# Kernel tuning notes

Measured on AMD Instinct MI355X. Metric: run time of the kernel, lower is better.

The kernel has to match this reference:

```python
import jax, jax.numpy as jnp
import numpy as np

FEATURE_DIM = 128
NUM_EDGES = 640000
NUM_NODES = 40000


def setup_inputs() -> dict:
    key = jax.random.key(0)
    ks = jax.random.split(key, 10)
    d = FEATURE_DIM
    scale = 1.0 / np.sqrt(d)
    inp = {
        "messages": jax.random.normal(ks[0], (NUM_EDGES, d), dtype=jnp.float32),
        "receivers": jax.random.randint(ks[1], (NUM_EDGES,), 0, NUM_NODES, dtype=jnp.int32),
        "num_segments": NUM_NODES,
        "Wk": jax.random.normal(ks[2], (d, d), dtype=jnp.float32) * scale,
        "bk": jnp.zeros((d,), dtype=jnp.float32),
        "Wv": jax.random.normal(ks[3], (d, d), dtype=jnp.float32) * scale,
        "bv": jnp.zeros((d,), dtype=jnp.float32),
        "Wq": jax.random.normal(ks[4], (d, d), dtype=jnp.float32) * scale,
        "bq": jnp.zeros((d,), dtype=jnp.float32),
        "Wo": jax.random.normal(ks[5], (d, d), dtype=jnp.float32) * scale,
        "bo": jnp.zeros((d,), dtype=jnp.float32),
    }
    return inp


def reference(messages, receivers, num_segments, Wk, bk, Wv, bv, Wq, bq, Wo, bo):
    d = messages.shape[-1]
    # per-edge key/value projections
    keys = messages @ Wk + bk            # [E, d]
    values = messages @ Wv + bv          # [E, d]
    # node-level summed messages -> queries
    summed = jax.ops.segment_sum(messages, receivers, num_segments)  # [N, d]
    queries = summed @ Wq + bq                                       # [N, d]
    # scalar attention score per edge (dot over full feature dim)
    msg_q = queries[receivers]                                       # [E, d]
    scores = jnp.sum(msg_q * keys, axis=-1) / jnp.sqrt(jnp.float32(d))  # [E]
    # segment softmax over edges sharing a receiver
    max_s = jax.ops.segment_max(scores, receivers, num_segments)     # [N]
    exp_s = jnp.exp(scores - max_s[receivers])                       # [E]
    sum_e = jax.ops.segment_sum(exp_s, receivers, num_segments)      # [N]
    attn = exp_s / (sum_e[receivers] + 1e-08)                        # [E]
    # weighted scatter-sum of values, then output projection
    agg = jax.ops.segment_sum(values * attn[:, None], receivers, num_segments)  # [N, d]
    return agg @ Wo + bo
```

## Files before the change

kernel.cpp:

```cpp
#include <hip/hip_runtime.h>

#define D 128
#define RSQRT_D 0.088388347648318440550f
#define NEG_HUGE -3.4e38f

#define FMA4(acc, s, b) { acc.x += (s)*(b).x; acc.y += (s)*(b).y; acc.z += (s)*(b).z; acc.w += (s)*(b).w; }

__global__ __launch_bounds__(256) void prep_kernel(
    const float* __restrict__ Wq, const float* __restrict__ Wk,
    const float* __restrict__ bq, const float* __restrict__ bk,
    const float* __restrict__ Wv, const float* __restrict__ Wo,
    const float* __restrict__ bv,
    float* __restrict__ Wqk, float* __restrict__ bqk,
    float* __restrict__ wqb, float* __restrict__ bqb,
    float* __restrict__ Wvo, float* __restrict__ bvo,
    int* __restrict__ zbase, int zcount) {
    int bid = blockIdx.x, t = threadIdx.x;
    if (bid < 64) {
        int i = bid * 2 + (t >> 7), j = t & 127;
        float a1 = 0.f, a2 = 0.f;
        for (int u = 0; u < D; ++u) {
            a1 += Wq[i * D + u] * Wk[j * D + u];
            a2 += Wv[i * D + u] * Wo[u * D + j];
        }
        Wqk[i * D + j] = a1;
        Wvo[i * D + j] = a2;
    } else if (bid == 64) {
        if (t < D) {
            int j = t;
            float a1 = 0.f, a2 = 0.f, a3 = 0.f;
            for (int u = 0; u < D; ++u) {
                a1 += bq[u] * Wk[j * D + u];
                a2 += Wq[j * D + u] * bk[u];
                a3 += bv[u] * Wo[u * D + j];
            }
            bqk[j] = a1; wqb[j] = a2; bvo[j] = a3;
            if (j == 0) {
                float b = 0.f;
                for (int u = 0; u < D; ++u) b += bq[u] * bk[u];
                *bqb = b;
            }
        }
    } else {
        int idx = (bid - 65) * 256 + t;
        if (idx < zcount) zbase[idx] = 0;
    }
}

__global__ void hist_kernel(const int* __restrict__ recv, int* __restrict__ cnt, int E) {
    int e = blockIdx.x * blockDim.x + threadIdx.x;
    if (e >= E) return;
    atomicAdd(&cnt[recv[e]], 1);
}

__global__ __launch_bounds__(1024) void scan_kernel(const int* __restrict__ cnt,
                                                    int* __restrict__ start, int N) {
    __shared__ int wsum[16];
    __shared__ int chunk_total;
    int t = threadIdx.x;
    int w = t >> 6, lane = t & 63;
    int running = 0;
    for (int base = 0; base <= N; base += 1024) {
        int i = base + t;
        int v = (i < N) ? cnt[i] : 0;
        int x = v;
#pragma unroll
        for (int off = 1; off < 64; off <<= 1) {
            int y = __shfl_up(x, off);
            if (lane >= off) x += y;
        }
        if (lane == 63) wsum[w] = x;
        __syncthreads();
        if (w == 0 && lane < 16) {
            int s = wsum[lane];
#pragma unroll
            for (int off = 1; off < 16; off <<= 1) {
                int y = __shfl_up(s, off);
                if (lane >= off) s += y;
            }
            wsum[lane] = s;
            if (lane == 15) chunk_total = s;
        }
        __syncthreads();
        int waveoff = (w == 0) ? 0 : wsum[w - 1];
        if (i <= N) start[i] = running + waveoff + x - v;
        running += chunk_total;
        __syncthreads();
    }
}

__global__ void fill_kernel(const int* __restrict__ recv, const int* __restrict__ start,
                            int* __restrict__ cursor, int* __restrict__ eidx, int E) {
    int e = blockIdx.x * blockDim.x + threadIdx.x;
    if (e >= E) return;
    int r = recv[e];
    int p = atomicAdd(&cursor[r], 1);
    eidx[start[r] + p] = e;
}

__global__ __launch_bounds__(256, 4) void mega_kernel(
    const float* __restrict__ msg, const int* __restrict__ eidx,
    const int* __restrict__ start,
    const float* __restrict__ Wqk, const float* __restrict__ bqk,
    const float* __restrict__ wqb, const float* __restrict__ bqbp,
    const float* __restrict__ Wvo, const float* __restrict__ bvo,
    const float* __restrict__ bo,
    float* __restrict__ out, int N) {
    __shared__ float4 sums4[16 * 32];
    __shared__ float4 qks4[16 * 32];
    __shared__ float sat[16];
    float* sums = (float*)sums4;

    int t = threadIdx.x;
    int lane = t & 63, w = t >> 6;
    int h = lane >> 5;
    int k = lane & 31;
    int base = blockIdx.x * 16;
    const float4* msg4 = (const float4*)msg;

    for (int b = 0; b < 4; ++b) {
        int n = base + w * 4 + b;
        int nl = n - base;
        int s0 = 0, s1 = 0;
        if (n < N) { s0 = start[n]; s1 = start[n + 1]; }
        float4 a0 = make_float4(0.f, 0.f, 0.f, 0.f);
        float4 a1 = make_float4(0.f, 0.f, 0.f, 0.f);
        int j = s0;
        for (; j + 4 <= s1; j += 4) {
            int eA = eidx[j + h];
            int eB = eidx[j + 2 + h];
            float4 fA = msg4[(size_t)eA * 32 + k];
            float4 fB = msg4[(size_t)eB * 32 + k];
            a0.x += fA.x; a0.y += fA.y; a0.z += fA.z; a0.w += fA.w;
            a1.x += fB.x; a1.y += fB.y; a1.z += fB.z; a1.w += fB.w;
        }
        for (; j < s1; j += 2) {
            int idx = j + h;
            int e = eidx[idx < s1 ? idx : s1 - 1];
            float4 f = msg4[(size_t)e * 32 + k];
            float mk = (idx < s1) ? 1.f : 0.f;
            a0.x += f.x * mk; a0.y += f.y * mk; a0.z += f.z * mk; a0.w += f.w * mk;
        }
        float4 a = make_float4(a0.x + a1.x, a0.y + a1.y, a0.z + a1.z, a0.w + a1.w);
        a.x += __shfl_xor(a.x, 32);
        a.y += __shfl_xor(a.y, 32);
        a.z += __shfl_xor(a.z, 32);
        a.w += __shfl_xor(a.w, 32);
        if (lane < 32 && n < N) sums4[nl * 32 + k] = a;
    }
    __syncthreads();

    {
        int c = t & 31, slot = t >> 5;
        const float4* B4 = (const float4*)Wqk;
        float4 acc0 = ((const float4*)bqk)[c];
        float4 acc1 = acc0;
        for (int i = 0; i < D; i += 4) {
            float4 aA = sums4[slot * 32 + (i >> 2)];
            float4 aB = sums4[(slot + 8) * 32 + (i >> 2)];
            float4 b0 = B4[(i + 0) * 32 + c];
            float4 b1 = B4[(i + 1) * 32 + c];
            float4 b2 = B4[(i + 2) * 32 + c];
            float4 b3 = B4[(i + 3) * 32 + c];
            FMA4(acc0, aA.x, b0); FMA4(acc0, aA.y, b1); FMA4(acc0, aA.z, b2); FMA4(acc0, aA.w, b3);
            FMA4(acc1, aB.x, b0); FMA4(acc1, aB.y, b1); FMA4(acc1, aB.z, b2); FMA4(acc1, aB.w, b3);
        }
        qks4[slot * 32 + c] = acc0;
        qks4[(slot + 8) * 32 + c] = acc1;
    }
    __syncthreads();

    float bqb = bqbp[0];
    for (int b = 0; b < 4; ++b) {
        int n = base + w * 4 + b;
        if (n >= N) break;
        int nl = n - base;
        int s0 = start[n], s1 = start[n + 1];
        float4 q = qks4[nl * 32 + k];
        float4 sv = sums4[nl * 32 + k];
        float4 wv = ((const float4*)wqb)[k];
        float pq = sv.x * wv.x + sv.y * wv.y + sv.z * wv.z + sv.w * wv.w;
        pq += __shfl_xor(pq, 1); pq += __shfl_xor(pq, 2); pq += __shfl_xor(pq, 4);
        pq += __shfl_xor(pq, 8); pq += __shfl_xor(pq, 16);
        float qb = pq + bqb;

        float m = NEG_HUGE, s = 0.f;
        float4 acc = make_float4(0.f, 0.f, 0.f, 0.f);
        int j = s0;
        float4 fC = make_float4(0.f, 0.f, 0.f, 0.f);
        if (j < s1) {
            int idx = j + h;
            int e = eidx[idx < s1 ? idx : s1 - 1];
            fC = msg4[(size_t)e * 32 + k];
        }
        while (j < s1) {
            int jn = j + 2;
            float4 fN = make_float4(0.f, 0.f, 0.f, 0.f);
            if (jn < s1) {
                int idx = jn + h;
                int e = eidx[idx < s1 ? idx : s1 - 1];
                fN = msg4[(size_t)e * 32 + k];
            }
            int valid = (j + h) < s1;
            float p = fC.x * q.x + fC.y * q.y + fC.z * q.z + fC.w * q.w;
            p += __shfl_xor(p, 1); p += __shfl_xor(p, 2); p += __shfl_xor(p, 4);
            p += __shfl_xor(p, 8); p += __shfl_xor(p, 16);
            float sc = valid ? (p + qb) * RSQRT_D : NEG_HUGE;
            float nm = fmaxf(m, sc);
            float scale = __expf(m - nm);
            float ww = __expf(sc - nm);
            s = s * scale + ww;
            acc.x = acc.x * scale + ww * fC.x;
            acc.y = acc.y * scale + ww * fC.y;
            acc.z = acc.z * scale + ww * fC.z;
            acc.w = acc.w * scale + ww * fC.w;
            m = nm;
            fC = fN;
            j = jn;
        }
        float mo = __shfl_xor(m, 32);
        float so = __shfl_xor(s, 32);
        float4 ao;
        ao.x = __shfl_xor(acc.x, 32); ao.y = __shfl_xor(acc.y, 32);
        ao.z = __shfl_xor(acc.z, 32); ao.w = __shfl_xor(acc.w, 32);
        float mt = fmaxf(m, mo);
        float c0 = __expf(m - mt), c1 = __expf(mo - mt);
        float st = s * c0 + so * c1;
        float4 aT;
        aT.x = acc.x * c0 + ao.x * c1;
        aT.y = acc.y * c0 + ao.y * c1;
        aT.z = acc.z * c0 + ao.z * c1;
        aT.w = acc.w * c0 + ao.w * c1;
        float inv = 1.f / (st + 1e-8f);
        if (lane < 32)
            sums4[nl * 32 + k] = make_float4(aT.x * inv, aT.y * inv, aT.z * inv, aT.w * inv);
        if (lane == 0) sat[nl] = st * inv;
    }
    __syncthreads();

    {
        int c = t & 31, slot = t >> 5;
        const float4* B4 = (const float4*)Wvo;
        float4 bo4 = ((const float4*)bo)[c];
        float4 bv4 = ((const float4*)bvo)[c];
        float sa0 = sat[slot], sa1 = sat[slot + 8];
        float4 acc0 = make_float4(bo4.x + sa0 * bv4.x, bo4.y + sa0 * bv4.y,
                                  bo4.z + sa0 * bv4.z, bo4.w + sa0 * bv4.w);
        float4 acc1 = make_float4(bo4.x + sa1 * bv4.x, bo4.y + sa1 * bv4.y,
                                  bo4.z + sa1 * bv4.z, bo4.w + sa1 * bv4.w);
        for (int i = 0; i < D; i += 4) {
            float4 aA = sums4[slot * 32 + (i >> 2)];
            float4 aB = sums4[(slot + 8) * 32 + (i >> 2)];
            float4 b0 = B4[(i + 0) * 32 + c];
            float4 b1 = B4[(i + 1) * 32 + c];
            float4 b2 = B4[(i + 2) * 32 + c];
            float4 b3 = B4[(i + 3) * 32 + c];
            FMA4(acc0, aA.x, b0); FMA4(acc0, aA.y, b1); FMA4(acc0, aA.z, b2); FMA4(acc0, aA.w, b3);
            FMA4(acc1, aB.x, b0); FMA4(acc1, aB.y, b1); FMA4(acc1, aB.z, b2); FMA4(acc1, aB.w, b3);
        }
        int n0 = base + slot, n1 = base + slot + 8;
        if (n0 < N) ((float4*)(out + (size_t)n0 * D))[c] = acc0;
        if (n1 < N) ((float4*)(out + (size_t)n1 * D))[c] = acc1;
    }
}


extern "C" void kernel_launch(void* const* d_in, const int* in_sizes, int n_in,
                              void* d_out, int out_size, void* d_ws, size_t ws_size,
                              hipStream_t stream) {
    const float* msg = (const float*)d_in[0];
    const int* recv = (const int*)d_in[1];
    const float* Wk = (const float*)d_in[3];
    const float* bk = (const float*)d_in[4];
    const float* Wv = (const float*)d_in[5];
    const float* bv = (const float*)d_in[6];
    const float* Wq = (const float*)d_in[7];
    const float* bq = (const float*)d_in[8];
    const float* Wo = (const float*)d_in[9];
    const float* bo = (const float*)d_in[10];
    float* out = (float*)d_out;

    int E = in_sizes[0] / D;
    int N = out_size / D;

    char* wsb = (char*)d_ws;
    size_t o = 0;
    auto alloc = [&](size_t elems) { void* p = wsb + o; o += elems * 4; return p; };

    int* cnt    = (int*)alloc(N);
    int* cursor = (int*)alloc(N);
    int* start  = (int*)alloc(N + 1);
    int* eidx   = (int*)alloc(E);
    float* Wqk  = (float*)alloc(D * D);
    float* bqk  = (float*)alloc(D);
    float* wqb  = (float*)alloc(D);
    float* bqb  = (float*)alloc(1);
    float* Wvo  = (float*)alloc(D * D);
    float* bvo  = (float*)alloc(D);

    int zcount = 2 * N;
    int zblocks = (zcount + 255) / 256;
    prep_kernel<<<65 + zblocks, 256, 0, stream>>>(Wq, Wk, bq, bk, Wv, Wo, bv,
                                                  Wqk, bqk, wqb, bqb, Wvo, bvo,
                                                  cnt, zcount);
    int nbE = (E + 255) / 256;
    hist_kernel<<<nbE, 256, 0, stream>>>(recv, cnt, E);
    scan_kernel<<<1, 1024, 0, stream>>>(cnt, start, N);
    fill_kernel<<<nbE, 256, 0, stream>>>(recv, start, cursor, eidx, E);
    mega_kernel<<<(N + 15) / 16, 256, 0, stream>>>(msg, eidx, start, Wqk, bqk, wqb, bqb,
                                                   Wvo, bvo, bo, out, N);
}
```

Before: 695.8 us.

## Stage gathered edge messages in LDS once and reuse across both passes

The fused node kernel now gathers each wave's edge message rows into shared memory once, using global_load_lds asynchronous copies, holding up to 70 edges per wave. Both the segment-sum pass and the softmax/aggregation pass read from this cache and fall back to global memory for overflow rows, so each message is fetched from global memory once instead of twice. Blocks shrink to 128 threads and 8 nodes to fit the roughly 72KB LDS cache, which limits occupancy to about one block per CU and drops the software prefetch in the softmax loop. The scan kernel is also vectorised to int4 loads and stores with prefetching, and workspace allocations are 64-byte aligned so those int4 accesses are aligned.

After: 753.6 us. +8.3%, slower.

```diff
diff --git a/kernel.cpp b/kernel.cpp
--- a/kernel.cpp
+++ b/kernel.cpp
@@ -3,8 +3,14 @@
 #define D 128
 #define RSQRT_D 0.088388347648318440550f
 #define NEG_HUGE -3.4e38f
+#define CAPW 70
 
 #define FMA4(acc, s, b) { acc.x += (s)*(b).x; acc.y += (s)*(b).y; acc.z += (s)*(b).z; acc.w += (s)*(b).w; }
+
+__device__ __forceinline__ void gld_lds16(const void* g, void* l) {
+    __builtin_amdgcn_global_load_lds((const __attribute__((address_space(1))) void*)g,
+                                     (__attribute__((address_space(3))) void*)l, 16, 0, 0);
+}
 
 __global__ __launch_bounds__(256) void prep_kernel(
     const float* __restrict__ Wq, const float* __restrict__ Wk,
@@ -60,10 +66,21 @@
     int t = threadIdx.x;
     int w = t >> 6, lane = t & 63;
     int running = 0;
-    for (int base = 0; base <= N; base += 1024) {
-        int i = base + t;
-        int v = (i < N) ? cnt[i] : 0;
-        int x = v;
+    const int4* cnt4 = (const int4*)cnt;
+    int nIter = (N + 4095) >> 12;
+    int4 v = make_int4(0, 0, 0, 0);
+    {
+        int i = t << 2;
+        if (i < N) v = cnt4[i >> 2];
+    }
+    for (int it = 0; it < nIter; ++it) {
+        int4 vn = make_int4(0, 0, 0, 0);
+        {
+            int i = ((it + 1) << 12) + (t << 2);
+            if (it + 1 < nIter && i < N) vn = cnt4[i >> 2];
+        }
+        int s0 = v.x, s1 = s0 + v.y, s2 = s1 + v.z, s3 = s2 + v.w;
+        int x = s3;
 #pragma unroll
         for (int off = 1; off < 64; off <<= 1) {
             int y = __shfl_up(x, off);
@@ -83,10 +100,14 @@
         }
         __syncthreads();
         int waveoff = (w == 0) ? 0 : wsum[w - 1];
-        if (i <= N) start[i] = running + waveoff + x - v;
+        int tb = running + waveoff + (x - s3);
+        int i = (it << 12) + (t << 2);
+        if (i < N) ((int4*)start)[i >> 2] = make_int4(tb, tb + s0, tb + s1, tb + s2);
         running += chunk_total;
         __syncthreads();
-    }
+        v = vn;
+    }
+    if (t == 0) start[N] = running;
 }
 
 __global__ void fill_kernel(const int* __restrict__ recv, const int* __restrict__ start,
@@ -98,7 +119,7 @@
     eidx[start[r] + p] = e;
 }
 
-__global__ __launch_bounds__(256, 4) void mega_kernel(
+__global__ __launch_bounds__(128, 1) void mega_kernel(
     const float* __restrict__ msg, const int* __restrict__ eidx,
     const int* __restrict__ start,
     const float* __restrict__ Wqk, const float* __restrict__ bqk,
@@ -106,47 +127,56 @@
     const float* __restrict__ Wvo, const float* __restrict__ bvo,
     const float* __restrict__ bo,
     float* __restrict__ out, int N) {
-    __shared__ float4 sums4[16 * 32];
-    __shared__ float4 qks4[16 * 32];
-    __shared__ float sat[16];
-    float* sums = (float*)sums4;
+    __shared__ float4 cache4[2 * CAPW * 32];
+    __shared__ float4 sums4[8 * 32];
+    __shared__ float4 qks4[8 * 32];
+    __shared__ float sat[8];
 
     int t = threadIdx.x;
     int lane = t & 63, w = t >> 6;
     int h = lane >> 5;
     int k = lane & 31;
-    int base = blockIdx.x * 16;
+    int base = blockIdx.x * 8;
     const float4* msg4 = (const float4*)msg;
 
+    int n0 = base + w * 4;
+    int sw0 = start[min(n0, N)];
+    int sw1 = start[min(n0 + 4, N)];
+    int Tw = sw1 - sw0;
+    int Tc = min(Tw, CAPW);
+
+    int e0 = (lane < Tc) ? eidx[sw0 + lane] : 0;
+    int e1 = (lane + 64 < Tc) ? eidx[sw0 + 64 + lane] : 0;
+    float* cbase = (float*)&cache4[w * CAPW * 32];
+    int npairs = (Tc + 1) >> 1;
+    for (int p = 0; p < npairs; ++p) {
+        int row = 2 * p + h;
+        int rr = min(row, Tc - 1);
+        int e = (rr < 64) ? __shfl(e0, rr) : __shfl(e1, rr - 64);
+        gld_lds16(msg + (size_t)e * D + (k << 2), cbase + p * 256);
+    }
+    asm volatile("s_waitcnt vmcnt(0)" ::: "memory");
+
     for (int b = 0; b < 4; ++b) {
-        int n = base + w * 4 + b;
+        int n = n0 + b;
+        if (n >= N) break;
         int nl = n - base;
-        int s0 = 0, s1 = 0;
-        if (n < N) { s0 = start[n]; s1 = start[n + 1]; }
-        float4 a0 = make_float4(0.f, 0.f, 0.f, 0.f);
-        float4 a1 = make_float4(0.f, 0.f, 0.f, 0.f);
-        int j = s0;
-        for (; j + 4 <= s1; j += 4) {
-            int eA = eidx[j + h];
-            int eB = eidx[j + 2 + h];
-            float4 fA = msg4[(size_t)eA * 32 + k];
-            float4 fB = msg4[(size_t)eB * 32 + k];
-            a0.x += fA.x; a0.y += fA.y; a0.z += fA.z; a0.w += fA.w;
-            a1.x += fB.x; a1.y += fB.y; a1.z += fB.z; a1.w += fB.w;
-        }
-        for (; j < s1; j += 2) {
-            int idx = j + h;
-            int e = eidx[idx < s1 ? idx : s1 - 1];
-            float4 f = msg4[(size_t)e * 32 + k];
-            float mk = (idx < s1) ? 1.f : 0.f;
-            a0.x += f.x * mk; a0.y += f.y * mk; a0.z += f.z * mk; a0.w += f.w * mk;
-        }
-        float4 a = make_float4(a0.x + a1.x, a0.y + a1.y, a0.z + a1.z, a0.w + a1.w);
+        int q0 = start[n] - sw0, q1 = start[n + 1] - sw0;
+        float4 a = make_float4(0.f, 0.f, 0.f, 0.f);
+        for (int j = q0; j < q1; j += 2) {
+            int row = j + h;
+            int rr = min(row, q1 - 1);
+            float4 f;
+            if (rr < Tc) f = cache4[(w * CAPW + rr) * 32 + k];
+            else f = msg4[(size_t)eidx[sw0 + rr] * 32 + k];
+            float mk = (row < q1) ? 1.f : 0.f;
+            a.x += f.x * mk; a.y += f.y * mk; a.z += f.z * mk; a.w += f.w * mk;
+        }
         a.x += __shfl_xor(a.x, 32);
         a.y += __shfl_xor(a.y, 32);
         a.z += __shfl_xor(a.z, 32);
         a.w += __shfl_xor(a.w, 32);
-        if (lane < 32 && n < N) sums4[nl * 32 + k] = a;
+        if (lane < 32) sums4[nl * 32 + k] = a;
     }
     __syncthreads();
 
@@ -157,7 +187,7 @@
         float4 acc1 = acc0;
         for (int i = 0; i < D; i += 4) {
             float4 aA = sums4[slot * 32 + (i >> 2)];
-            float4 aB = sums4[(slot + 8) * 32 + (i >> 2)];
+            float4 aB = sums4[(slot + 4) * 32 + (i >> 2)];
             float4 b0 = B4[(i + 0) * 32 + c];
             float4 b1 = B4[(i + 1) * 32 + c];
             float4 b2 = B4[(i + 2) * 32 + c];
@@ -166,16 +196,16 @@
             FMA4(acc1, aB.x, b0); FMA4(acc1, aB.y, b1); FMA4(acc1, aB.z, b2); FMA4(acc1, aB.w, b3);
         }
         qks4[slot * 32 + c] = acc0;
-        qks4[(slot + 8) * 32 + c] = acc1;
+        qks4[(slot + 4) * 32 + c] = acc1;
     }
     __syncthreads();
 
     float bqb = bqbp[0];
     for (int b = 0; b < 4; ++b) {
-        int n = base + w * 4 + b;
+        int n = n0 + b;
         if (n >= N) break;
         int nl = n - base;
-        int s0 = start[n], s1 = start[n + 1];
+        int q0 = start[n] - sw0, q1 = start[n + 1] - sw0;
         float4 q = qks4[nl * 32 + k];
         float4 sv = sums4[nl * 32 + k];
         float4 wv = ((const float4*)wqb)[k];
@@ -186,23 +216,14 @@
 
         float m = NEG_HUGE, s = 0.f;
         float4 acc = make_float4(0.f, 0.f, 0.f, 0.f);
-        int j = s0;
-        float4 fC = make_float4(0.f, 0.f, 0.f, 0.f);
-        if (j < s1) {
-            int idx = j + h;
-            int e = eidx[idx < s1 ? idx : s1 - 1];
-            fC = msg4[(size_t)e * 32 + k];
-        }
-        while (j < s1) {
-            int jn = j + 2;
-            float4 fN = make_float4(0.f, 0.f, 0.f, 0.f);
-            if (jn < s1) {
-                int idx = jn + h;
-                int e = eidx[idx < s1 ? idx : s1 - 1];
-                fN = msg4[(size_t)e * 32 + k];
-            }
-            int valid = (j + h) < s1;
-            float p = fC.x * q.x + fC.y * q.y + fC.z * q.z + fC.w * q.w;
+        for (int j = q0; j < q1; j += 2) {
+            int row = j + h;
+            int rr = min(row, q1 - 1);
+            float4 f;
+            if (rr < Tc) f = cache4[(w * CAPW + rr) * 32 + k];
+            else f = msg4[(size_t)eidx[sw0 + rr] * 32 + k];
+            int valid = row < q1;
+            float p = f.x * q.x + f.y * q.y + f.z * q.z + f.w * q.w;
             p += __shfl_xor(p, 1); p += __shfl_xor(p, 2); p += __shfl_xor(p, 4);
             p += __shfl_xor(p, 8); p += __shfl_xor(p, 16);
             float sc = valid ? (p + qb) * RSQRT_D : NEG_HUGE;
@@ -210,13 +231,11 @@
             float scale = __expf(m - nm);
             float ww = __expf(sc - nm);
             s = s * scale + ww;
-            acc.x = acc.x * scale + ww * fC.x;
-            acc.y = acc.y * scale + ww * fC.y;
-            acc.z = acc.z * scale + ww * fC.z;
-            acc.w = acc.w * scale + ww * fC.w;
+            acc.x = acc.x * scale + ww * f.x;
+            acc.y = acc.y * scale + ww * f.y;
+            acc.z = acc.z * scale + ww * f.z;
+            acc.w = acc.w * scale + ww * f.w;
             m = nm;
-            fC = fN;
-            j = jn;
         }
         float mo = __shfl_xor(m, 32);
         float so = __shfl_xor(s, 32);
@@ -243,14 +262,14 @@
         const float4* B4 = (const float4*)Wvo;
         float4 bo4 = ((const float4*)bo)[c];
         float4 bv4 = ((const float4*)bvo)[c];
-        float sa0 = sat[slot], sa1 = sat[slot + 8];
+        float sa0 = sat[slot], sa1 = sat[slot + 4];
         float4 acc0 = make_float4(bo4.x + sa0 * bv4.x, bo4.y + sa0 * bv4.y,
                                   bo4.z + sa0 * bv4.z, bo4.w + sa0 * bv4.w);
         float4 acc1 = make_float4(bo4.x + sa1 * bv4.x, bo4.y + sa1 * bv4.y,
                                   bo4.z + sa1 * bv4.z, bo4.w + sa1 * bv4.w);
         for (int i = 0; i < D; i += 4) {
             float4 aA = sums4[slot * 32 + (i >> 2)];
-            float4 aB = sums4[(slot + 8) * 32 + (i >> 2)];
+            float4 aB = sums4[(slot + 4) * 32 + (i >> 2)];
             float4 b0 = B4[(i + 0) * 32 + c];
             float4 b1 = B4[(i + 1) * 32 + c];
             float4 b2 = B4[(i + 2) * 32 + c];
@@ -258,9 +277,9 @@
             FMA4(acc0, aA.x, b0); FMA4(acc0, aA.y, b1); FMA4(acc0, aA.z, b2); FMA4(acc0, aA.w, b3);
             FMA4(acc1, aB.x, b0); FMA4(acc1, aB.y, b1); FMA4(acc1, aB.z, b2); FMA4(acc1, aB.w, b3);
         }
-        int n0 = base + slot, n1 = base + slot + 8;
-        if (n0 < N) ((float4*)(out + (size_t)n0 * D))[c] = acc0;
-        if (n1 < N) ((float4*)(out + (size_t)n1 * D))[c] = acc1;
+        int nA = base + slot, nB = base + slot + 4;
+        if (nA < N) ((float4*)(out + (size_t)nA * D))[c] = acc0;
+        if (nB < N) ((float4*)(out + (size_t)nB * D))[c] = acc1;
     }
 }
 
@@ -285,7 +304,11 @@
 
     char* wsb = (char*)d_ws;
     size_t o = 0;
-    auto alloc = [&](size_t elems) { void* p = wsb + o; o += elems * 4; return p; };
+    auto alloc = [&](size_t elems) {
+        void* p = wsb + o;
+        o += (elems * 4 + 63) & ~(size_t)63;
+        return p;
+    };
 
     int* cnt    = (int*)alloc(N);
     int* cursor = (int*)alloc(N);
@@ -307,6 +330,6 @@
     hist_kernel<<<nbE, 256, 0, stream>>>(recv, cnt, E);
     scan_kernel<<<1, 1024, 0, stream>>>(cnt, start, N);
     fill_kernel<<<nbE, 256, 0, stream>>>(recv, start, cursor, eidx, E);
-    mega_kernel<<<(N + 15) / 16, 256, 0, stream>>>(msg, eidx, start, Wqk, bqk, wqb, bqb,
-                                                   Wvo, bvo, bo, out, N);
-}
+    mega_kernel<<<(N + 7) / 8, 128, 0, stream>>>(msg, eidx, start, Wqk, bqk, wqb, bqb,
+                                                 Wvo, bvo, bo, out, N);
+}
```
